# Performance work log

Hardware: AMD Instinct MI355X
Metric: run time of the kernel (lower is better)

The kernel has to match this reference:

```python
import jax, jax.numpy as jnp
import numpy as np

N_HEAD = 16

def setup_inputs() -> dict:
    key = jax.random.key(0)
    k1, k2, k3 = jax.random.split(key, 3)
    B, T, C = 2, 2048, 1024
    x_norm_for_qk = jax.random.normal(k1, (B, T, C), dtype=jnp.float32)
    xt_current_for_v = jax.random.normal(k2, (B, T, C), dtype=jnp.float32)
    W_attn = jax.random.normal(k3, (C, 2 * C), dtype=jnp.float32) * (1.0 / np.sqrt(C))
    b_attn = jnp.zeros((2 * C,), dtype=jnp.float32)
    return {"x_norm_for_qk": x_norm_for_qk, "xt_current_for_v": xt_current_for_v,
            "W_attn": W_attn, "b_attn": b_attn}

def reference(x_norm_for_qk, xt_current_for_v, W_attn, b_attn):
    B, T, C = x_norm_for_qk.shape
    H = N_HEAD
    D = C // H  # head dim
    qk = x_norm_for_qk @ W_attn + b_attn          # [B,T,2C]
    q, k = qk[..., :C], qk[..., C:]
    q = q.reshape(B, T, H, D).transpose(0, 2, 1, 3)   # [B,H,T,D]
    k = k.reshape(B, T, H, D).transpose(0, 2, 1, 3)
    v = xt_current_for_v.reshape(B, T, H, D).transpose(0, 2, 1, 3)
    scale = 1.0 / np.sqrt(D).astype(np.float32)
    scores = jnp.einsum('bhqd,bhkd->bhqk', q, k) * scale  # [B,H,T,T]
    causal = jnp.tril(jnp.ones((T, T), dtype=bool))
    scores = jnp.where(causal[None, None], scores, jnp.float32(-jnp.inf))
    weights = jax.nn.softmax(scores, axis=-1)  # dropout p=0.0 -> identity
    y = jnp.einsum('bhqk,bhkd->bhqd', weights, v)
    return y.transpose(0, 2, 1, 3).reshape(B, T, C)
```

## Files before the change

### kernel.cpp

```cpp
#include <hip/hip_runtime.h>
#include <hip/hip_bf16.h>
#include <math.h>

typedef __attribute__((ext_vector_type(8))) short s8v;
typedef __attribute__((ext_vector_type(4))) float f4v;
typedef __attribute__((ext_vector_type(16))) float f16v;
typedef unsigned short ush;
typedef unsigned int u32;

#define QSCALE 0.180336880f

static __device__ __forceinline__ ush f2bf(float f) {
    u32 x = __builtin_bit_cast(u32, f);
    return (ush)((x + 0x7fffu + ((x >> 16) & 1u)) >> 16);
}
static __device__ __forceinline__ u32 bfpack(float lo, float hi) {
    u32 a = __builtin_bit_cast(u32, lo) + 0x8000u;
    u32 b = __builtin_bit_cast(u32, hi) + 0x8000u;
    return __builtin_amdgcn_perm(b, a, 0x07060302);
}
static __device__ __forceinline__ void gl_lds16(const void* g, void* l) {
    __builtin_amdgcn_global_load_lds(
        (const __attribute__((address_space(1))) u32*)g,
        (__attribute__((address_space(3))) u32*)l, 16, 0, 0);
}
#if __has_builtin(__builtin_amdgcn_exp2f)
#define EXP2F(x) __builtin_amdgcn_exp2f(x)
#else
#define EXP2F(x) exp2f(x)
#endif

__global__ __launch_bounds__(256) void prepA_kernel(
    const float* __restrict__ X, const float* __restrict__ W,
    ush* __restrict__ Xb, ush* __restrict__ Wt)
{
    __shared__ float Ts[64][68];
    const int tid = threadIdx.x;
    const int bid = blockIdx.x;
    if (bid < 2048) {
        const size_t i = ((size_t)bid * 256 + tid) * 8;
        float4 v0 = *(const float4*)(X + i);
        float4 v1 = *(const float4*)(X + i + 4);
        uint4 o;
        o.x = bfpack(v0.x, v0.y); o.y = bfpack(v0.z, v0.w);
        o.z = bfpack(v1.x, v1.y); o.w = bfpack(v1.z, v1.w);
        *(uint4*)(Xb + i) = o;
    } else {
        const int id = bid - 2048;
        const int n0 = (id & 31) * 64, k0 = (id >> 5) * 64;
        #pragma unroll
        for (int p = 0; p < 4; ++p) {
            const int idx = p * 256 + tid;
            const int kr = idx >> 4, nc4 = idx & 15;
            float4 v = *(const float4*)(W + (size_t)(k0 + kr) * 2048 + n0 + nc4 * 4);
            Ts[kr][nc4 * 4 + 0] = v.x; Ts[kr][nc4 * 4 + 1] = v.y;
            Ts[kr][nc4 * 4 + 2] = v.z; Ts[kr][nc4 * 4 + 3] = v.w;
        }
        __syncthreads();
        const int n = tid >> 2, kb = (tid & 3) * 16;
        #pragma unroll
        for (int p = 0; p < 4; ++p) {
            const int k = kb + p * 4;
            ushort4 o;
            o.x = f2bf(Ts[k + 0][n]); o.y = f2bf(Ts[k + 1][n]);
            o.z = f2bf(Ts[k + 2][n]); o.w = f2bf(Ts[k + 3][n]);
            *(ushort4*)(Wt + (size_t)(n0 + n) * 1024 + k0 + k) = o;
        }
    }
}

__global__ __launch_bounds__(256) void vt_kernel(
    const float* __restrict__ XV, ush* __restrict__ Vt)
{
    __shared__ float Ts[64][68];
    const int tid = threadIdx.x;
    const int t0 = blockIdx.x * 64;
    const int bh = blockIdx.y;
    const int b = bh >> 4, h = bh & 15;
    #pragma unroll
    for (int p = 0; p < 4; ++p) {
        const int idx = p * 256 + tid;
        const int tr = idx >> 4, dc4 = idx & 15;
        float4 v = *(const float4*)(XV + (size_t)(b * 2048 + t0 + tr) * 1024
                                    + h * 64 + dc4 * 4);
        Ts[tr][dc4 * 4 + 0] = v.x; Ts[tr][dc4 * 4 + 1] = v.y;
        Ts[tr][dc4 * 4 + 2] = v.z; Ts[tr][dc4 * 4 + 3] = v.w;
    }
    __syncthreads();
    const int d = tid >> 2, tb = (tid & 3) * 16;
    #pragma unroll
    for (int p = 0; p < 4; ++p) {
        const int tq = tb + p * 4;
        ushort4 o;
        o.x = f2bf(Ts[tq + 0][d]); o.y = f2bf(Ts[tq + 1][d]);
        o.z = f2bf(Ts[tq + 2][d]); o.w = f2bf(Ts[tq + 3][d]);
        *(ushort4*)(Vt + (size_t)((b * 16 + h) * 64 + d) * 2048 + t0 + tq) = o;
    }
}

__global__ __launch_bounds__(256) void gemm_kernel(
    const ush* __restrict__ Xb, const ush* __restrict__ Wt,
    const float* __restrict__ bias,
    ush* __restrict__ Qb, ush* __restrict__ Kb)
{
    __shared__ ush As[128 * 32];
    __shared__ ush Bs[128 * 32];

    const int tid = threadIdx.x;
    const int wid = tid >> 6, lane = tid & 63;
    const int quad = lane >> 4, l15 = lane & 15;
    const int wm = wid >> 1, wn = wid & 1;
    const int m0 = blockIdx.y * 128, n0 = blockIdx.x * 128;

    const int lrow = lane >> 2;
    const int lkk = (lane & 3) * 8;
    const size_t arow = (size_t)(m0 + wid * 32 + lrow);
    const size_t brow = (size_t)(n0 + wid * 32 + lrow);
    ush* AsW = &As[wid * 1024];
    ush* BsW = &Bs[wid * 1024];

    f4v acc[4][4];
    #pragma unroll
    for (int i = 0; i < 4; ++i)
        #pragma unroll
        for (int j = 0; j < 4; ++j) acc[i][j] = (f4v){0.f, 0.f, 0.f, 0.f};

    for (int k0 = 0; k0 < 1024; k0 += 32) {
        gl_lds16(Xb + arow * 1024 + k0 + lkk, AsW);
        gl_lds16(Xb + (arow + 16) * 1024 + k0 + lkk, AsW + 512);
        gl_lds16(Wt + brow * 1024 + k0 + lkk, BsW);
        gl_lds16(Wt + (brow + 16) * 1024 + k0 + lkk, BsW + 512);
        __syncthreads();

        s8v a[4], bf[4];
        #pragma unroll
        for (int i = 0; i < 4; ++i)
            a[i] = *(const s8v*)&As[(wm * 64 + i * 16 + l15) * 32 + quad * 8];
        #pragma unroll
        for (int j = 0; j < 4; ++j)
            bf[j] = *(const s8v*)&Bs[(wn * 64 + j * 16 + l15) * 32 + quad * 8];
        #pragma unroll
        for (int i = 0; i < 4; ++i)
            #pragma unroll
            for (int j = 0; j < 4; ++j)
                acc[i][j] = __builtin_amdgcn_mfma_f32_16x16x32_bf16(
                    a[i], bf[j], acc[i][j], 0, 0, 0);
        __syncthreads();
    }

    #pragma unroll
    for (int j = 0; j < 4; ++j) {
        const int n = n0 + wn * 64 + j * 16 + l15;
        const float bv = bias[n];
        const bool is_k = n >= 1024;
        const int nn = n & 1023;
        const int h = nn >> 6, d = nn & 63;
        ush* dst = is_k ? Kb : Qb;
        #pragma unroll
        for (int i = 0; i < 4; ++i) {
            const int mrow = m0 + wm * 64 + i * 16 + quad * 4;
            #pragma unroll
            for (int r = 0; r < 4; ++r) {
                const int m = mrow + r;
                const int b = m >> 11, t = m & 2047;
                float val = acc[i][j][r] + bv;
                if (!is_k) val *= QSCALE;
                dst[(size_t)((b * 16 + h) * 2048 + t) * 64 + d] = f2bf(val);
            }
        }
    }
}

__global__ __launch_bounds__(256, 2) void attn_kernel(
    const ush* __restrict__ Qb, const ush* __restrict__ Kb,
    const ush* __restrict__ Vt, float* __restrict__ Y)
{
    __shared__ ush SMEM[25600];
    ush* Kbuf = SMEM;
    ush* Vbuf = SMEM + 8192;
    ush* Pq   = SMEM + 16384;

    const int tid = threadIdx.x;
    const int w = tid >> 6, lane = tid & 63;
    const int l31 = lane & 31, hi = lane >> 5;

    const int idx = blockIdx.x;
    const int half = idx >> 8, pair = idx & 255;
    const int qt = half ? (pair & 15) : 15 - (pair & 15);
    const int bh = (pair >> 4) + half * 16;
    const int b = bh >> 4, h = bh & 15;
    const int q0 = qt * 128;
    const int ktmax = 2 * qt + 1;

    const ush* Qg = Qb + (size_t)bh * 2048 * 64;
    const ush* Kg = Kb + (size_t)bh * 2048 * 64;
    const ush* Vg = Vt + (size_t)bh * 64 * 2048;

    ush* Pw = Pq + w * 2304;

    {
        const int r8 = lane >> 3, c8 = lane & 7;
        #pragma unroll
        for (int p = 0; p < 4; ++p) {
            const int row = p * 8 + r8;
            uint4 v = *(const uint4*)(Qg + (size_t)(q0 + w * 32 + row) * 64 + c8 * 8);
            *(uint4*)&Pw[row * 72 + c8 * 8] = v;
        }
    }
    s8v bq[4];
    #pragma unroll
    for (int s = 0; s < 4; ++s)
        bq[s] = *(const s8v*)&Pw[l31 * 72 + s * 16 + hi * 8];

    const int r8 = lane >> 3;
    const int g8 = ((lane & 7) ^ r8) * 8;
    auto stage = [&](int kt, int buf) {
        const int k0e = kt * 64;
        const ush* kg = Kg + (size_t)(k0e + w * 16 + r8) * 64 + g8;
        gl_lds16(kg, &Kbuf[buf * 4096 + (w * 16) * 64]);
        gl_lds16(kg + 8 * 64, &Kbuf[buf * 4096 + (w * 16 + 8) * 64]);
        const ush* vg = Vg + (size_t)(w * 16 + r8) * 2048 + k0e + g8;
        gl_lds16(vg, &Vbuf[buf * 4096 + (w * 16) * 64]);
        gl_lds16(vg + 8 * 2048, &Vbuf[buf * 4096 + (w * 16 + 8) * 64]);
    };

    f16v acco0 = {}, acco1 = {};
    float mr = -INFINITY, lr = 0.f;
    const int qg = q0 + w * 32 + l31;

    stage(0, 0);
    __syncthreads();

    for (int kt = 0; kt <= ktmax; ++kt) {
        const int buf = kt & 1;
        if (kt < ktmax) stage(kt + 1, buf ^ 1);

        f16v s0 = {}, s1 = {};
        #pragma unroll
        for (int s = 0; s < 4; ++s) {
            const int ch = (s << 1) + hi;
            const int row0 = l31, row1 = 32 + l31;
            s8v ak0 = *(const s8v*)&Kbuf[buf * 4096 + row0 * 64 + ((ch ^ (row0 & 7)) << 3)];
            s8v ak1 = *(const s8v*)&Kbuf[buf * 4096 + row1 * 64 + ((ch ^ (row1 & 7)) << 3)];
            s0 = __builtin_amdgcn_mfma_f32_32x32x16_bf16(ak0, bq[s], s0, 0, 0, 0);
            s1 = __builtin_amdgcn_mfma_f32_32x32x16_bf16(ak1, bq[s], s1, 0, 0, 0);
        }

        const bool needmask = (kt * 64 + 63) > (q0 + w * 32);
        float mloc = -INFINITY;
        #pragma unroll
        for (int r = 0; r < 16; ++r) {
            float v0 = s0[r], v1 = s1[r];
            if (needmask) {
                const int keyb = kt * 64 + (r & 3) + 8 * (r >> 2) + 4 * hi;
                if (keyb > qg) v0 = -INFINITY;
                if (keyb + 32 > qg) v1 = -INFINITY;
                s0[r] = v0; s1[r] = v1;
            }
            mloc = fmaxf(mloc, fmaxf(v0, v1));
        }
        mloc = fmaxf(mloc, __shfl_xor(mloc, 32));
        const float mnew = fmaxf(mr, mloc);
        const float alpha = EXP2F(mr - mnew);
        mr = mnew;

        float ps = 0.f;
        #pragma unroll
        for (int g4 = 0; g4 < 4; ++g4) {
            float e0a = EXP2F(s0[g4 * 4 + 0] - mnew), e0b = EXP2F(s0[g4 * 4 + 1] - mnew);
            float e0c = EXP2F(s0[g4 * 4 + 2] - mnew), e0d = EXP2F(s0[g4 * 4 + 3] - mnew);
            float e1a = EXP2F(s1[g4 * 4 + 0] - mnew), e1b = EXP2F(s1[g4 * 4 + 1] - mnew);
            float e1c = EXP2F(s1[g4 * 4 + 2] - mnew), e1d = EXP2F(s1[g4 * 4 + 3] - mnew);
            ps += (e0a + e0b) + (e0c + e0d) + (e1a + e1b) + (e1c + e1d);
            uint2 p0; p0.x = bfpack(e0a, e0b); p0.y = bfpack(e0c, e0d);
            uint2 p1; p1.x = bfpack(e1a, e1b); p1.y = bfpack(e1c, e1d);
            const int off = g4 * 8 + hi * 4;
            *(uint2*)&Pw[l31 * 72 + off] = p0;
            *(uint2*)&Pw[l31 * 72 + 32 + off] = p1;
        }
        ps += __shfl_xor(ps, 32);
        lr = lr * alpha + ps;

        #pragma unroll
        for (int r = 0; r < 16; ++r) { acco0[r] *= alpha; acco1[r] *= alpha; }

        #pragma unroll
        for (int s = 0; s < 4; ++s) {
            s8v pf = *(const s8v*)&Pw[l31 * 72 + s * 16 + hi * 8];
            const int ch = (s << 1) + hi;
            const int row0 = l31, row1 = 32 + l31;
            s8v av0 = *(const s8v*)&Vbuf[buf * 4096 + row0 * 64 + ((ch ^ (row0 & 7)) << 3)];
            s8v av1 = *(const s8v*)&Vbuf[buf * 4096 + row1 * 64 + ((ch ^ (row1 & 7)) << 3)];
            acco0 = __builtin_amdgcn_mfma_f32_32x32x16_bf16(av0, pf, acco0, 0, 0, 0);
            acco1 = __builtin_amdgcn_mfma_f32_32x32x16_bf16(av1, pf, acco1, 0, 0, 0);
        }

        __syncthreads();
    }

    __syncthreads();
    float* LTw = (float*)SMEM + w * (32 * 68);
    const float inv = 1.0f / lr;
    #pragma unroll
    for (int r = 0; r < 16; ++r) {
        const int d = (r & 3) + 8 * (r >> 2) + 4 * hi;
        LTw[l31 * 68 + d] = acco0[r] * inv;
        LTw[l31 * 68 + 32 + d] = acco1[r] * inv;
    }
    const int qr4 = lane >> 4, chk = lane & 15;
    #pragma unroll
    for (int p = 0; p < 8; ++p) {
        const int qrow = p * 4 + qr4;
        f4v v = *(const f4v*)&LTw[qrow * 68 + chk * 4];
        *(float4*)(Y + (size_t)(b * 2048 + q0 + w * 32 + qrow) * 1024
                   + h * 64 + chk * 4) = (float4){v[0], v[1], v[2], v[3]};
    }
}

extern "C" void kernel_launch(void* const* d_in, const int* in_sizes, int n_in,
                              void* d_out, int out_size, void* d_ws,
                              size_t ws_size, hipStream_t stream)
{
    const float* x_qk = (const float*)d_in[0];
    const float* x_v  = (const float*)d_in[1];
    const float* W    = (const float*)d_in[2];
    const float* bias = (const float*)d_in[3];
    float* out = (float*)d_out;

    unsigned char* ws = (unsigned char*)d_ws;
    ush* Xb = (ush*)(ws);
    ush* Vt = (ush*)(ws);
    ush* Wt = (ush*)(ws + (8u << 20));
    ush* Qb = (ush*)(ws + (12u << 20));
    ush* Kb = (ush*)(ws + (20u << 20));

    prepA_kernel<<<2560, 256, 0, stream>>>(x_qk, W, Xb, Wt);
    gemm_kernel<<<dim3(16, 32), 256, 0, stream>>>(Xb, Wt, bias, Qb, Kb);
    vt_kernel<<<dim3(32, 32), 256, 0, stream>>>(x_v, Vt);
    attn_kernel<<<512, 256, 0, stream>>>(Qb, Kb, Vt, out);
}
```

Measured before the change: 161.9 us.

## Software-pipeline QK^T one tile ahead, split K/V staging, add lazy rescale

```diff
diff --git a/kernel.cpp b/kernel.cpp
--- a/kernel.cpp
+++ b/kernel.cpp
@@ -199,10 +199,10 @@
     ush* Pw = Pq + w * 2304;
 
     {
-        const int r8 = lane >> 3, c8 = lane & 7;
+        const int r8q = lane >> 3, c8 = lane & 7;
         #pragma unroll
         for (int p = 0; p < 4; ++p) {
-            const int row = p * 8 + r8;
+            const int row = p * 8 + r8q;
             uint4 v = *(const uint4*)(Qg + (size_t)(q0 + w * 32 + row) * 64 + c8 * 8);
             *(uint4*)&Pw[row * 72 + c8 * 8] = v;
         }
@@ -214,11 +214,14 @@
 
     const int r8 = lane >> 3;
     const int g8 = ((lane & 7) ^ r8) * 8;
-    auto stage = [&](int kt, int buf) {
+    auto stageK = [&](int kt, int buf) {
         const int k0e = kt * 64;
         const ush* kg = Kg + (size_t)(k0e + w * 16 + r8) * 64 + g8;
         gl_lds16(kg, &Kbuf[buf * 4096 + (w * 16) * 64]);
         gl_lds16(kg + 8 * 64, &Kbuf[buf * 4096 + (w * 16 + 8) * 64]);
+    };
+    auto stageV = [&](int kt, int buf) {
+        const int k0e = kt * 64;
         const ush* vg = Vg + (size_t)(w * 16 + r8) * 2048 + k0e + g8;
         gl_lds16(vg, &Vbuf[buf * 4096 + (w * 16) * 64]);
         gl_lds16(vg + 8 * 2048, &Vbuf[buf * 4096 + (w * 16 + 8) * 64]);
@@ -228,22 +231,44 @@
     float mr = -INFINITY, lr = 0.f;
     const int qg = q0 + w * 32 + l31;
 
-    stage(0, 0);
+    stageK(0, 0); stageV(0, 0); stageK(1, 1);
+    __syncthreads();
+
+    f16v s0 = {}, s1 = {};
+    __builtin_amdgcn_s_setprio(1);
+    #pragma unroll
+    for (int s = 0; s < 4; ++s) {
+        const int ch = (s << 1) + hi;
+        const int row0 = l31, row1 = 32 + l31;
+        s8v ak0 = *(const s8v*)&Kbuf[row0 * 64 + ((ch ^ (row0 & 7)) << 3)];
+        s8v ak1 = *(const s8v*)&Kbuf[row1 * 64 + ((ch ^ (row1 & 7)) << 3)];
+        s0 = __builtin_amdgcn_mfma_f32_32x32x16_bf16(ak0, bq[s], s0, 0, 0, 0);
+        s1 = __builtin_amdgcn_mfma_f32_32x32x16_bf16(ak1, bq[s], s1, 0, 0, 0);
+    }
+    __builtin_amdgcn_s_setprio(0);
     __syncthreads();
 
     for (int kt = 0; kt <= ktmax; ++kt) {
         const int buf = kt & 1;
-        if (kt < ktmax) stage(kt + 1, buf ^ 1);
-
-        f16v s0 = {}, s1 = {};
-        #pragma unroll
-        for (int s = 0; s < 4; ++s) {
-            const int ch = (s << 1) + hi;
-            const int row0 = l31, row1 = 32 + l31;
-            s8v ak0 = *(const s8v*)&Kbuf[buf * 4096 + row0 * 64 + ((ch ^ (row0 & 7)) << 3)];
-            s8v ak1 = *(const s8v*)&Kbuf[buf * 4096 + row1 * 64 + ((ch ^ (row1 & 7)) << 3)];
-            s0 = __builtin_amdgcn_mfma_f32_32x32x16_bf16(ak0, bq[s], s0, 0, 0, 0);
-            s1 = __builtin_amdgcn_mfma_f32_32x32x16_bf16(ak1, bq[s], s1, 0, 0, 0);
+
+        if (kt < ktmax) {
+            stageV(kt + 1, buf ^ 1);
+            if (kt + 2 <= ktmax) stageK(kt + 2, buf);
+        }
+
+        f16v t0 = {}, t1 = {};
+        if (kt < ktmax) {
+            __builtin_amdgcn_s_setprio(1);
+            #pragma unroll
+            for (int s = 0; s < 4; ++s) {
+                const int ch = (s << 1) + hi;
+                const int row0 = l31, row1 = 32 + l31;
+                s8v ak0 = *(const s8v*)&Kbuf[(buf ^ 1) * 4096 + row0 * 64 + ((ch ^ (row0 & 7)) << 3)];
+                s8v ak1 = *(const s8v*)&Kbuf[(buf ^ 1) * 4096 + row1 * 64 + ((ch ^ (row1 & 7)) << 3)];
+                t0 = __builtin_amdgcn_mfma_f32_32x32x16_bf16(ak0, bq[s], t0, 0, 0, 0);
+                t1 = __builtin_amdgcn_mfma_f32_32x32x16_bf16(ak1, bq[s], t1, 0, 0, 0);
+            }
+            __builtin_amdgcn_s_setprio(0);
         }
 
         const bool needmask = (kt * 64 + 63) > (q0 + w * 32);
@@ -260,17 +285,23 @@
             mloc = fmaxf(mloc, fmaxf(v0, v1));
         }
         mloc = fmaxf(mloc, __shfl_xor(mloc, 32));
-        const float mnew = fmaxf(mr, mloc);
-        const float alpha = EXP2F(mr - mnew);
-        mr = mnew;
+
+        if (__any(mloc > mr + 8.0f)) {
+            const float mnew = fmaxf(mr, mloc);
+            const float alpha = EXP2F(mr - mnew);
+            #pragma unroll
+            for (int r = 0; r < 16; ++r) { acco0[r] *= alpha; acco1[r] *= alpha; }
+            lr *= alpha;
+            mr = mnew;
+        }
 
         float ps = 0.f;
         #pragma unroll
         for (int g4 = 0; g4 < 4; ++g4) {
-            float e0a = EXP2F(s0[g4 * 4 + 0] - mnew), e0b = EXP2F(s0[g4 * 4 + 1] - mnew);
-            float e0c = EXP2F(s0[g4 * 4 + 2] - mnew), e0d = EXP2F(s0[g4 * 4 + 3] - mnew);
-            float e1a = EXP2F(s1[g4 * 4 + 0] - mnew), e1b = EXP2F(s1[g4 * 4 + 1] - mnew);
-            float e1c = EXP2F(s1[g4 * 4 + 2] - mnew), e1d = EXP2F(s1[g4 * 4 + 3] - mnew);
+            float e0a = EXP2F(s0[g4 * 4 + 0] - mr), e0b = EXP2F(s0[g4 * 4 + 1] - mr);
+            float e0c = EXP2F(s0[g4 * 4 + 2] - mr), e0d = EXP2F(s0[g4 * 4 + 3] - mr);
+            float e1a = EXP2F(s1[g4 * 4 + 0] - mr), e1b = EXP2F(s1[g4 * 4 + 1] - mr);
+            float e1c = EXP2F(s1[g4 * 4 + 2] - mr), e1d = EXP2F(s1[g4 * 4 + 3] - mr);
             ps += (e0a + e0b) + (e0c + e0d) + (e1a + e1b) + (e1c + e1d);
             uint2 p0; p0.x = bfpack(e0a, e0b); p0.y = bfpack(e0c, e0d);
             uint2 p1; p1.x = bfpack(e1a, e1b); p1.y = bfpack(e1c, e1d);
@@ -279,11 +310,9 @@
             *(uint2*)&Pw[l31 * 72 + 32 + off] = p1;
         }
         ps += __shfl_xor(ps, 32);
-        lr = lr * alpha + ps;
-
-        #pragma unroll
-        for (int r = 0; r < 16; ++r) { acco0[r] *= alpha; acco1[r] *= alpha; }
-
+        lr += ps;
+
+        __builtin_amdgcn_s_setprio(1);
         #pragma unroll
         for (int s = 0; s < 4; ++s) {
             s8v pf = *(const s8v*)&Pw[l31 * 72 + s * 16 + hi * 8];
@@ -294,8 +323,10 @@
             acco0 = __builtin_amdgcn_mfma_f32_32x32x16_bf16(av0, pf, acco0, 0, 0, 0);
             acco1 = __builtin_amdgcn_mfma_f32_32x32x16_bf16(av1, pf, acco1, 0, 0, 0);
         }
+        __builtin_amdgcn_s_setprio(0);
 
         __syncthreads();
+        s0 = t0; s1 = t1;
     }
 
     __syncthreads();
```

Result: slower. 167.0 us (+3.1%).
